# Kernel optimization log

Hardware: AMD Instinct MI355X
Metric: run time of the kernel (lower is better)

## Reference

```python
import jax, jax.numpy as jnp
import numpy as np
import math

D_MODEL = 1024
N_HEADS = 16
FFN_DIM = 4096
B, L = 8, 1024
LN_EPS = 1e-5


def setup_inputs() -> dict:
    key = jax.random.key(0)
    ks = jax.random.split(key, 16)
    s = 1.0 / math.sqrt(D_MODEL)
    sf = 1.0 / math.sqrt(FFN_DIM)
    # weights stored [in, out] (transposed vs torch nn.Linear)
    return {
        "x": jax.random.normal(ks[0], (B, L, D_MODEL), dtype=jnp.float32),
        "Wq": jax.random.normal(ks[1], (D_MODEL, D_MODEL), dtype=jnp.float32) * s,
        "bq": jnp.zeros((D_MODEL,), jnp.float32),
        "Wk": jax.random.normal(ks[2], (D_MODEL, D_MODEL), dtype=jnp.float32) * s,
        "bk": jnp.zeros((D_MODEL,), jnp.float32),
        "Wv": jax.random.normal(ks[3], (D_MODEL, D_MODEL), dtype=jnp.float32) * s,
        "bv": jnp.zeros((D_MODEL,), jnp.float32),
        "Wo": jax.random.normal(ks[4], (D_MODEL, D_MODEL), dtype=jnp.float32) * s,
        "bo": jnp.zeros((D_MODEL,), jnp.float32),
        "W1": jax.random.normal(ks[5], (D_MODEL, FFN_DIM), dtype=jnp.float32) * s,
        "b1": jnp.zeros((FFN_DIM,), jnp.float32),
        "W2": jax.random.normal(ks[6], (FFN_DIM, D_MODEL), dtype=jnp.float32) * sf,
        "b2": jnp.zeros((D_MODEL,), jnp.float32),
        "gamma": jnp.ones((D_MODEL,), jnp.float32),
        "beta": jnp.zeros((D_MODEL,), jnp.float32),
    }


def reference(x, Wq, bq, Wk, bk, Wv, bv, Wo, bo, W1, b1, W2, b2, gamma, beta):
    Bb, Ll, D = x.shape
    H = N_HEADS
    E = D // H
    scale = 1.0 / math.sqrt(E)
    # multi-head attention (dropout is identity in eval)
    q = (x @ Wq + bq).reshape(Bb, Ll, H, E)
    k = (x @ Wk + bk).reshape(Bb, Ll, H, E)
    v = (x @ Wv + bv).reshape(Bb, Ll, H, E)
    scores = jnp.einsum('blhe,bshe->bhls', q, k)  # [B,H,L,L]
    A = jax.nn.softmax(scale * scores, axis=-1)
    ctx = jnp.einsum('bhls,bshd->blhd', A, v).reshape(Bb, Ll, D)
    attn_out = ctx @ Wo + bo
    x = x + attn_out
    # FFN: conv1d kernel_size=1 == pointwise linear; exact (erf) GELU as in F.gelu
    h = jax.nn.gelu(x @ W1 + b1, approximate=False)
    x = x + (h @ W2 + b2)
    # LayerNorm
    mu = jnp.mean(x, axis=-1, keepdims=True)
    var = jnp.mean(jnp.square(x - mu), axis=-1, keepdims=True)
    out = (x - mu) * jax.lax.rsqrt(var + LN_EPS) * gamma + beta
    return out
```

## Files before the change

### kernel.cpp

```cpp
#include <hip/hip_runtime.h>
#include <cmath>

typedef __attribute__((ext_vector_type(8))) _Float16 half8;
typedef __attribute__((ext_vector_type(4))) _Float16 half4;
typedef __attribute__((ext_vector_type(4))) float f32x4;

__device__ __forceinline__ void glds16(const void* g, void* l) {
  __builtin_amdgcn_global_load_lds(
      (__attribute__((address_space(1))) const void*)g,
      (__attribute__((address_space(3))) void*)l, 16, 0, 0);
}

__device__ __forceinline__ float fast_erf(float x) {
  float ax = fabsf(x);
  float t = 1.0f / (1.0f + 0.3275911f * ax);
  float y = t * (0.254829592f +
            t * (-0.284496736f +
            t * (1.421413741f +
            t * (-1.453152027f + t * 1.061405429f))));
  float r = 1.0f - y * __expf(-ax * ax);
  return copysignf(r, x);
}

__global__ __launch_bounds__(256) void k_cvt(const float* __restrict__ in,
                                             _Float16* __restrict__ out) {
  int i = (blockIdx.x * 256 + threadIdx.x) * 8;
  const f32x4* p = (const f32x4*)(in + i);
  f32x4 a = p[0], b = p[1];
  half8 h;
  h[0] = (_Float16)a[0]; h[1] = (_Float16)a[1]; h[2] = (_Float16)a[2]; h[3] = (_Float16)a[3];
  h[4] = (_Float16)b[0]; h[5] = (_Float16)b[1]; h[6] = (_Float16)b[2]; h[7] = (_Float16)b[3];
  *(half8*)(out + i) = h;
}

__global__ __launch_bounds__(256) void k_wt(const float* __restrict__ W,
                                            _Float16* __restrict__ Wt, int K, int N) {
  __shared__ float t[32][33];
  int x = threadIdx.x & 31, y4 = (threadIdx.x >> 5) << 2;
  int n0 = blockIdx.x << 5, k0 = blockIdx.y << 5;
#pragma unroll
  for (int r = 0; r < 4; ++r) t[y4 + r][x] = W[(size_t)(k0 + y4 + r) * N + n0 + x];
  __syncthreads();
#pragma unroll
  for (int r = 0; r < 4; ++r) Wt[(size_t)(n0 + y4 + r) * K + k0 + x] = (_Float16)t[x][y4 + r];
}

__global__ void k_biascat(const float* __restrict__ a, const float* __restrict__ b,
                          const float* __restrict__ c, float* __restrict__ o) {
  int i = blockIdx.x * 256 + threadIdx.x;
  const float* s = i < 1024 ? a : (i < 2048 ? b : c);
  o[i] = s[i & 1023];
}

template <int BM, int EPI>
__global__ __launch_bounds__(512, 2) void k_gemm8(
    const _Float16* __restrict__ A, const _Float16* __restrict__ Bt,
    const float* __restrict__ bias, const float* __restrict__ res,
    float* __restrict__ outf, _Float16* __restrict__ outh, int M, int N, int K) {
  constexpr int MR = BM / 32;
  constexpr int MH2 = MR / 2;
  constexpr int AL = BM * 64;
  constexpr int BL = 256 * 64;
  constexpr int ABYTES = BM * 128;
  constexpr int BBYTES = 256 * 128;
  constexpr int AB2 = 2 * ABYTES;
  __shared__ _Float16 lds[2 * (AL + BL)];
  const char* ldsc = (const char*)lds;

  const int tid = threadIdx.x;
  const int lane = tid & 63;
  const int w = tid >> 6, wr = w >> 2, wc = w & 3;
  const int l15 = lane & 15, grp = lane >> 4;

  const int gx = gridDim.x;
  const int nwg = gx * gridDim.y;
  const int lid = blockIdx.y * gx + blockIdx.x;
  const int wid = (lid & 7) * (nwg >> 3) + (lid >> 3);
  const int m0 = (wid / gx) * BM, n0 = (wid % gx) * 256;

  const int m2 = (l15 >> 2) & 1, m01 = l15 & 3;
  const int chunk0 = (m2 << 2) | (grp ^ m01);
  const int aoff0 = wr * 2048 + l15 * 128 + chunk0 * 16;
  const int aoff1 = aoff0 ^ 64;
  const int boff0 = wc * 2048 + l15 * 128 + chunk0 * 16;
  const int boff1 = boff0 ^ 64;

  const int srow = tid >> 3;
  const int scs8 = ((tid & 7) ^ (srow & 7)) * 8;
  const int NK = K >> 6;

  f32x4 acc[MR][4] = {};
  half8 af[MH2][2], bf[2][2];

#define STG_A(J, MHH, KN)                                                      \
  _Pragma("unroll") for (int s = 0; s < BM / 128; ++s)                         \
      glds16(A + (size_t)(m0 + (MHH) * (BM / 2) + s * 64 + srow) * K +         \
                 (size_t)(KN)*64 + scs8,                                       \
             lds + (J)*AL + ((MHH) * (BM / 2) + s * 64) * 64 + tid * 8);
#define STG_B(J, NHH, KN)                                                      \
  _Pragma("unroll") for (int s = 0; s < 2; ++s)                                \
      glds16(Bt + (size_t)(n0 + (NHH)*128 + s * 64 + srow) * K +               \
                  (size_t)(KN)*64 + scs8,                                      \
             lds + 2 * AL + (J)*BL + ((NHH)*128 + s * 64) * 64 + tid * 8);

#define STG_ALL(J, KN)                                                         \
  STG_A(J, 0, KN) STG_B(J, 0, KN) STG_B(J, 1, KN) STG_A(J, 1, KN)

#define VM_A                                                                   \
  do {                                                                         \
    if constexpr (BM == 256) asm volatile("s_waitcnt vmcnt(8)" ::: "memory");  \
    else asm volatile("s_waitcnt vmcnt(6)" ::: "memory");                      \
  } while (0)
#define VM_B                                                                   \
  do {                                                                         \
    if constexpr (BM == 256) asm volatile("s_waitcnt vmcnt(4)" ::: "memory");  \
    else asm volatile("s_waitcnt vmcnt(3)" ::: "memory");                      \
  } while (0)
#define VM_NONE

#define PHASE(J, MHQ, NHQ, RA, RB, STGSTMT, VMSTMT)                            \
  {                                                                            \
    if constexpr (RA) {                                                        \
      _Pragma("unroll") for (int i = 0; i < MH2; ++i) {                        \
        af[i][0] = *(const half8*)(ldsc + (J)*ABYTES +                         \
                                   ((MHQ)*MH2 + i) * 4096 + aoff0);            \
        af[i][1] = *(const half8*)(ldsc + (J)*ABYTES +                         \
                                   ((MHQ)*MH2 + i) * 4096 + aoff1);            \
      }                                                                        \
    }                                                                          \
    if constexpr (RB) {                                                        \
      _Pragma("unroll") for (int n = 0; n < 2; ++n) {                          \
        bf[n][0] = *(const half8*)(ldsc + AB2 + (J)*BBYTES +                   \
                                   ((NHQ)*2 + n) * 8192 + boff0);              \
        bf[n][1] = *(const half8*)(ldsc + AB2 + (J)*BBYTES +                   \
                                   ((NHQ)*2 + n) * 8192 + boff1);              \
      }                                                                        \
    }                                                                          \
    STGSTMT;                                                                   \
    __builtin_amdgcn_s_barrier();                                              \
    __builtin_amdgcn_s_setprio(1);                                             \
    _Pragma("unroll") for (int ks = 0; ks < 2; ++ks)                           \
        _Pragma("unroll") for (int i = 0; i < MH2; ++i)                        \
            _Pragma("unroll") for (int n = 0; n < 2; ++n)                      \
                acc[(MHQ)*MH2 + i][(NHQ)*2 + n] =                              \
                    __builtin_amdgcn_mfma_f32_16x16x32_f16(                    \
                        af[i][ks], bf[n][ks], acc[(MHQ)*MH2 + i][(NHQ)*2 + n], \
                        0, 0, 0);                                              \
    __builtin_amdgcn_s_setprio(0);                                             \
    VMSTMT;                                                                    \
    __builtin_amdgcn_s_barrier();                                              \
  }

#define KTILE(J, KT)                                                           \
  {                                                                            \
    const int kn_ = ((KT) + 1 < NK) ? (KT) + 1 : (KT);                         \
    PHASE(J, 0, 0, true, true, STG_ALL(1 - (J), kn_), VM_A)                    \
    PHASE(J, 0, 1, false, true, , VM_NONE)                                     \
    PHASE(J, 1, 1, true, false, , VM_NONE)                                     \
    PHASE(J, 1, 0, false, true, , VM_B)                                        \
  }

  STG_ALL(0, 0)
  VM_B;
  __builtin_amdgcn_s_barrier();

#pragma unroll 1
  for (int kt = 0; kt < NK; kt += 2) {
    KTILE(0, kt)
    KTILE(1, kt + 1)
  }
  asm volatile("s_waitcnt vmcnt(0)" ::: "memory");
#undef KTILE
#undef PHASE
#undef VM_A
#undef VM_B
#undef VM_NONE
#undef STG_ALL
#undef STG_A
#undef STG_B

  float bcol[4];
#pragma unroll
  for (int n = 0; n < 4; ++n) bcol[n] = bias[n0 + (n * 4 + wc) * 16 + l15];
#pragma unroll
  for (int m = 0; m < MR; ++m) {
#pragma unroll
    for (int rr = 0; rr < 4; ++rr) {
      const size_t row = m0 + (m * 2 + wr) * 16 + grp * 4 + rr;
#pragma unroll
      for (int n = 0; n < 4; ++n) {
        const int col = n0 + (n * 4 + wc) * 16 + l15;
        float v = acc[m][n][rr] + bcol[n];
        const size_t idx = row * N + col;
        if (EPI == 0) {
          outh[idx] = (_Float16)v;
        } else if (EPI == 1) {
          float t2 = v + res[idx];
          outf[idx] = t2;
          outh[idx] = (_Float16)t2;
        } else if (EPI == 2) {
          float g = 0.5f * v * (1.0f + fast_erf(v * 0.70710678118654752f));
          outh[idx] = (_Float16)g;
        } else {
          outf[idx] = v + res[idx];
        }
      }
    }
  }
}

__global__ __launch_bounds__(256) void k_vt(const _Float16* __restrict__ qkv,
                                            _Float16* __restrict__ Vt) {
  __shared__ _Float16 t[64 * 66];
  const int tid = threadIdx.x;
  const int bh = blockIdx.y, b = bh >> 4, h = bh & 15;
  const int s0 = blockIdx.x << 6;
#pragma unroll
  for (int p = 0; p < 2; ++p) {
    int lin = p * 256 + tid;
    int s = lin >> 3, c8 = lin & 7;
    half8 v = *(const half8*)&qkv[(size_t)(b * 1024 + s0 + s) * 3072 + 2048 + h * 64 + c8 * 8];
    union { half8 h8; unsigned u[4]; } u;
    u.h8 = v;
    unsigned* d = (unsigned*)&t[s * 66 + c8 * 8];
#pragma unroll
    for (int k = 0; k < 4; ++k) d[k] = u.u[k];
  }
  __syncthreads();
#pragma unroll
  for (int p = 0; p < 2; ++p) {
    int lin = p * 256 + tid;
    int e = lin >> 3, c8 = lin & 7;
    half8 v;
#pragma unroll
    for (int j = 0; j < 8; ++j) v[j] = t[(c8 * 8 + j) * 66 + e];
    *(half8*)&Vt[(size_t)(bh * 64 + e) * 1024 + s0 + c8 * 8] = v;
  }
}

__global__ __launch_bounds__(256) void k_attn(const _Float16* __restrict__ qkv,
                                              const _Float16* __restrict__ Vt,
                                              _Float16* __restrict__ ctx) {
  __shared__ _Float16 Ks[128 * 64];
  __shared__ _Float16 Vs[64 * 128];
  __shared__ _Float16 Ps[4][16 * 136];
  const int tid = threadIdx.x;
  const int lane = tid & 63, w = tid >> 6;
  const int l15 = lane & 15, grp = lane >> 4;
  const int bh = blockIdx.y, b = bh >> 4, h = bh & 15;
  const int q0 = blockIdx.x << 6;
  const float CSC = 0.125f * 1.44269504088896f;

  half8 qf[2];
  {
    const _Float16* qp = qkv + (size_t)(b * 1024 + q0 + w * 16 + l15) * 3072 + h * 64 + grp * 8;
    qf[0] = *(const half8*)qp;
    qf[1] = *(const half8*)(qp + 32);
  }
  f32x4 octx[4] = {};
  float mrun = -1e30f, lrun = 0.f;

  for (int kt = 0; kt < 8; ++kt) {
    const int s0 = kt * 128;
#pragma unroll
    for (int i = 0; i < 4; ++i) {
      {
        int srow = i * 32 + (tid >> 3);
        int c8 = (tid & 7) ^ (srow & 7);
        glds16(qkv + (size_t)(b * 1024 + s0 + srow) * 3072 + 1024 + h * 64 + c8 * 8,
               Ks + w * 512 + i * 2048);
      }
      {
        int erow = i * 16 + (tid >> 4);
        int c16 = (tid & 15) ^ (erow & 7);
        glds16(Vt + (size_t)(bh * 64 + erow) * 1024 + s0 + c16 * 8,
               Vs + w * 512 + i * 2048);
      }
    }
    __syncthreads();
    f32x4 sacc[8] = {};
#pragma unroll
    for (int ks = 0; ks < 2; ++ks)
#pragma unroll
      for (int f = 0; f < 8; ++f) {
        int srow = f * 16 + l15;
        half8 kf = *(const half8*)&Ks[srow * 64 + ((ks * 32 + grp * 8) ^ ((srow & 7) * 8))];
        sacc[f] = __builtin_amdgcn_mfma_f32_16x16x32_f16(kf, qf[ks], sacc[f], 0, 0, 0);
      }
    float sv[8][4];
    float tmax = -1e30f;
#pragma unroll
    for (int f = 0; f < 8; ++f)
#pragma unroll
      for (int r = 0; r < 4; ++r) {
        float v = sacc[f][r] * CSC;
        sv[f][r] = v;
        tmax = fmaxf(tmax, v);
      }
    tmax = fmaxf(tmax, __shfl_xor(tmax, 16));
    tmax = fmaxf(tmax, __shfl_xor(tmax, 32));
    float mnew = fmaxf(mrun, tmax);
    float corr = exp2f(mrun - mnew);
    float tsum = 0.f;
#pragma unroll
    for (int f = 0; f < 8; ++f)
#pragma unroll
      for (int r = 0; r < 4; ++r) {
        float pv = exp2f(sv[f][r] - mnew);
        sv[f][r] = pv;
        tsum += pv;
      }
    tsum += __shfl_xor(tsum, 16);
    tsum += __shfl_xor(tsum, 32);
    lrun = lrun * corr + tsum;
    mrun = mnew;
#pragma unroll
    for (int r = 0; r < 4; ++r) {
      float cq = __shfl(corr, (lane & 48) + grp * 4 + r);
#pragma unroll
      for (int jf = 0; jf < 4; ++jf) octx[jf][r] *= cq;
    }
#pragma unroll
    for (int f = 0; f < 8; ++f) {
      half4 pk;
      pk[0] = (_Float16)sv[f][0]; pk[1] = (_Float16)sv[f][1];
      pk[2] = (_Float16)sv[f][2]; pk[3] = (_Float16)sv[f][3];
      *(half4*)&Ps[w][l15 * 136 + f * 16 + grp * 4] = pk;
    }
#pragma unroll
    for (int ks2 = 0; ks2 < 4; ++ks2) {
      half8 pa = *(const half8*)&Ps[w][l15 * 136 + ks2 * 32 + grp * 8];
#pragma unroll
      for (int jf = 0; jf < 4; ++jf) {
        int erow = jf * 16 + l15;
        half8 vb = *(const half8*)&Vs[erow * 128 + ((ks2 * 32 + grp * 8) ^ ((erow & 7) * 8))];
        octx[jf] = __builtin_amdgcn_mfma_f32_16x16x32_f16(pa, vb, octx[jf], 0, 0, 0);
      }
    }
    __syncthreads();
  }
#pragma unroll
  for (int r = 0; r < 4; ++r) {
    float lq = __shfl(lrun, (lane & 48) + grp * 4 + r);
    float inv = 1.0f / lq;
    const size_t row = b * 1024 + q0 + w * 16 + grp * 4 + r;
#pragma unroll
    for (int jf = 0; jf < 4; ++jf)
      ctx[row * 1024 + h * 64 + jf * 16 + l15] = (_Float16)(octx[jf][r] * inv);
  }
}

__global__ __launch_bounds__(256) void k_ln(const float* xin, const float* __restrict__ gamma,
                                            const float* __restrict__ beta, float* out) {
  __shared__ float red[8];
  const int tid = threadIdx.x;
  const size_t row = blockIdx.x;
  f32x4 v = *(const f32x4*)&xin[row * 1024 + tid * 4];
  float s = v[0] + v[1] + v[2] + v[3];
  float s2 = v[0] * v[0] + v[1] * v[1] + v[2] * v[2] + v[3] * v[3];
#pragma unroll
  for (int o = 32; o >= 1; o >>= 1) {
    s += __shfl_xor(s, o);
    s2 += __shfl_xor(s2, o);
  }
  if ((tid & 63) == 0) { red[tid >> 6] = s; red[4 + (tid >> 6)] = s2; }
  __syncthreads();
  s = red[0] + red[1] + red[2] + red[3];
  s2 = red[4] + red[5] + red[6] + red[7];
  float mu = s * (1.0f / 1024.0f);
  float var = s2 * (1.0f / 1024.0f) - mu * mu;
  float rs = rsqrtf(var + 1e-5f);
  f32x4 g = *(const f32x4*)&gamma[tid * 4];
  f32x4 bt = *(const f32x4*)&beta[tid * 4];
  f32x4 o4;
#pragma unroll
  for (int r = 0; r < 4; ++r) o4[r] = (v[r] - mu) * rs * g[r] + bt[r];
  *(f32x4*)&out[row * 1024 + tid * 4] = o4;
}

extern "C" void kernel_launch(void* const* d_in, const int* in_sizes, int n_in,
                              void* d_out, int out_size, void* d_ws, size_t ws_size,
                              hipStream_t stream) {
  (void)in_sizes; (void)n_in; (void)out_size; (void)ws_size;
  const float* x  = (const float*)d_in[0];
  const float* Wq = (const float*)d_in[1];  const float* bq = (const float*)d_in[2];
  const float* Wk = (const float*)d_in[3];  const float* bk = (const float*)d_in[4];
  const float* Wv = (const float*)d_in[5];  const float* bv = (const float*)d_in[6];
  const float* Wo = (const float*)d_in[7];  const float* bo = (const float*)d_in[8];
  const float* W1 = (const float*)d_in[9];  const float* b1 = (const float*)d_in[10];
  const float* W2 = (const float*)d_in[11]; const float* b2 = (const float*)d_in[12];
  const float* gamma = (const float*)d_in[13];
  const float* beta  = (const float*)d_in[14];
  float* out = (float*)d_out;

  char* p = (char*)d_ws;
  _Float16* xb    = (_Float16*)p;  p += (size_t)16 << 20;
  _Float16* qkv   = (_Float16*)p;
  _Float16* hbuf  = (_Float16*)p;  p += (size_t)48 << 20;
  _Float16* Vt    = (_Float16*)p;  p += (size_t)16 << 20;
  _Float16* Wqkvt = (_Float16*)p;  p += (size_t)3072 * 1024 * 2;
  _Float16* Wot   = (_Float16*)p;  p += (size_t)1024 * 1024 * 2;
  _Float16* W1t   = (_Float16*)p;  p += (size_t)4096 * 1024 * 2;
  _Float16* W2t   = (_Float16*)p;  p += (size_t)4096 * 1024 * 2;
  float*    bqkv  = (float*)p;     p += (size_t)3072 * 4;
  float*    x1    = (float*)p;     p += (size_t)32 << 20;
  _Float16* x1b   = (_Float16*)p;  p += (size_t)16 << 20;
  _Float16* ctx   = xb;

  k_cvt<<<4096, 256, 0, stream>>>(x, xb);
  k_wt<<<dim3(32, 32), 256, 0, stream>>>(Wq, Wqkvt, 1024, 1024);
  k_wt<<<dim3(32, 32), 256, 0, stream>>>(Wk, Wqkvt + 1024 * 1024, 1024, 1024);
  k_wt<<<dim3(32, 32), 256, 0, stream>>>(Wv, Wqkvt + 2048 * 1024, 1024, 1024);
  k_wt<<<dim3(32, 32), 256, 0, stream>>>(Wo, Wot, 1024, 1024);
  k_wt<<<dim3(128, 32), 256, 0, stream>>>(W1, W1t, 1024, 4096);
  k_wt<<<dim3(32, 128), 256, 0, stream>>>(W2, W2t, 4096, 1024);
  k_biascat<<<12, 256, 0, stream>>>(bq, bk, bv, bqkv);

  k_gemm8<128, 0><<<dim3(12, 64), 512, 0, stream>>>(xb, Wqkvt, bqkv, nullptr, nullptr, qkv,
                                                    8192, 3072, 1024);
  k_vt<<<dim3(16, 128), 256, 0, stream>>>(qkv, Vt);
  k_attn<<<dim3(16, 128), 256, 0, stream>>>(qkv, Vt, ctx);
  k_gemm8<128, 1><<<dim3(4, 64), 512, 0, stream>>>(ctx, Wot, bo, x, x1, x1b, 8192, 1024, 1024);
  k_gemm8<256, 2><<<dim3(16, 32), 512, 0, stream>>>(x1b, W1t, b1, nullptr, nullptr, hbuf,
                                                    8192, 4096, 1024);
  k_gemm8<128, 3><<<dim3(4, 64), 512, 0, stream>>>(hbuf, W2t, b2, x1, out, nullptr,
                                                   8192, 1024, 4096);
  k_ln<<<8192, 256, 0, stream>>>(out, gamma, beta, out);
}
```

Before: 380.0 us.

## Add triple-buffered 256x128 GEMM kernel for QKV, out-proj and FFN2

Introduces k_gemmf, a 256x128-tile GEMM with three LDS stages and a two-tile-ahead global-to-LDS prefetch, two workgroups per CU, and an XCD-aware block remap. It replaces the older 128-row k_gemm8 for the QKV, output-projection and second FFN GEMMs. The aim is deeper load/compute overlap and better L2 locality. It also adds an explicit lgkmcnt wait and sched_barrier before the MFMA block, and hardcodes the vmcnt waits in the existing kernel to the BM=256 values. That kernel is now only instantiated with BM=256, so the hardcoding is consistent. The larger LDS footprint and the extra waits could limit occupancy or add stalls.

```diff
diff --git a/kernel.cpp b/kernel.cpp
--- a/kernel.cpp
+++ b/kernel.cpp
@@ -106,16 +106,8 @@
 #define STG_ALL(J, KN)                                                         \
   STG_A(J, 0, KN) STG_B(J, 0, KN) STG_B(J, 1, KN) STG_A(J, 1, KN)
 
-#define VM_A                                                                   \
-  do {                                                                         \
-    if constexpr (BM == 256) asm volatile("s_waitcnt vmcnt(8)" ::: "memory");  \
-    else asm volatile("s_waitcnt vmcnt(6)" ::: "memory");                      \
-  } while (0)
-#define VM_B                                                                   \
-  do {                                                                         \
-    if constexpr (BM == 256) asm volatile("s_waitcnt vmcnt(4)" ::: "memory");  \
-    else asm volatile("s_waitcnt vmcnt(3)" ::: "memory");                      \
-  } while (0)
+#define VM_A asm volatile("s_waitcnt vmcnt(8)" ::: "memory")
+#define VM_B asm volatile("s_waitcnt vmcnt(4)" ::: "memory")
 #define VM_NONE
 
 #define PHASE(J, MHQ, NHQ, RA, RB, STGSTMT, VMSTMT)                            \
@@ -138,6 +130,8 @@
     }                                                                          \
     STGSTMT;                                                                   \
     __builtin_amdgcn_s_barrier();                                              \
+    asm volatile("s_waitcnt lgkmcnt(0)");                                      \
+    __builtin_amdgcn_sched_barrier(0);                                         \
     __builtin_amdgcn_s_setprio(1);                                             \
     _Pragma("unroll") for (int ks = 0; ks < 2; ++ks)                           \
         _Pragma("unroll") for (int i = 0; i < MH2; ++i)                        \
@@ -209,6 +203,124 @@
   }
 }
 
+template <int EPI>
+__global__ __launch_bounds__(512, 2) void k_gemmf(
+    const _Float16* __restrict__ A, const _Float16* __restrict__ Bt,
+    const float* __restrict__ bias, const float* __restrict__ res,
+    float* __restrict__ outf, _Float16* __restrict__ outh, int M, int N, int K) {
+  constexpr int AL = 256 * 64, BL = 128 * 64;
+  constexpr int ABY = 32768, BBY = 16384, BBASE = 3 * ABY;
+  __shared__ _Float16 lds[3 * (AL + BL)];
+  const char* ldsc = (const char*)lds;
+
+  const int tid = threadIdx.x;
+  const int lane = tid & 63;
+  const int w = tid >> 6, wr = w >> 1, wc = w & 1;
+  const int l15 = lane & 15, grp = lane >> 4;
+
+  const int gx = gridDim.x;
+  const int nwg = gx * gridDim.y;
+  const int lid = blockIdx.y * gx + blockIdx.x;
+  const int wid = (lid & 7) * (nwg >> 3) + (lid >> 3);
+  const int m0 = (wid / gx) * 256, n0 = (wid % gx) * 128;
+
+  const int m2 = (l15 >> 2) & 1, m01 = l15 & 3;
+  const int c0 = ((m2 << 2) | (grp ^ m01)) * 16;
+  const int aoff0 = wr * 2048 + l15 * 128 + c0;
+  const int aoff1 = aoff0 ^ 64;
+  const int boff0 = wc * 2048 + l15 * 128 + c0;
+  const int boff1 = boff0 ^ 64;
+
+  const int srow = tid >> 3;
+  const int scs8 = ((tid & 7) ^ (srow & 7)) * 8;
+  const int NK = K >> 6;
+
+  const _Float16* aG = A + (size_t)(m0 + srow) * K + scs8;
+  const _Float16* bG = Bt + (size_t)(n0 + srow) * K + scs8;
+
+  f32x4 acc[4][4] = {};
+
+#define FSTG_A(JJ, HH, KN)                                                     \
+  _Pragma("unroll") for (int s = 0; s < 2; ++s)                                \
+      glds16(aG + (size_t)((HH)*128 + s * 64) * K + (size_t)(KN)*64,           \
+             lds + (JJ)*AL + ((HH)*128 + s * 64) * 64 + tid * 8);
+#define FSTG_B(JJ, HH, KN)                                                     \
+  glds16(bG + (size_t)((HH)*64) * K + (size_t)(KN)*64,                         \
+         lds + 3 * AL + (JJ)*BL + (HH)*64 * 64 + tid * 8);
+
+#define FPHASE(PA, PB, AO, BO, STGSTMT, VMSTMT)                                \
+  {                                                                            \
+    half8 af_[4], bf_[4];                                                      \
+    _Pragma("unroll") for (int m = 0; m < 4; ++m)                              \
+        af_[m] = *(const half8*)((PA) + m * 8192 + (AO));                      \
+    _Pragma("unroll") for (int n = 0; n < 4; ++n)                              \
+        bf_[n] = *(const half8*)((PB) + n * 4096 + (BO));                      \
+    STGSTMT;                                                                   \
+    __builtin_amdgcn_s_barrier();                                              \
+    asm volatile("s_waitcnt lgkmcnt(0)");                                      \
+    __builtin_amdgcn_sched_barrier(0);                                         \
+    __builtin_amdgcn_s_setprio(1);                                             \
+    _Pragma("unroll") for (int m = 0; m < 4; ++m)                              \
+        _Pragma("unroll") for (int n = 0; n < 4; ++n)                          \
+            acc[m][n] = __builtin_amdgcn_mfma_f32_16x16x32_f16(                \
+                af_[m], bf_[n], acc[m][n], 0, 0, 0);                           \
+    __builtin_amdgcn_s_setprio(0);                                             \
+    VMSTMT;                                                                    \
+    __builtin_amdgcn_s_barrier();                                              \
+  }
+
+  FSTG_A(0, 0, 0) FSTG_A(0, 1, 0) FSTG_B(0, 0, 0) FSTG_B(0, 1, 0)
+  FSTG_A(1, 0, 1) FSTG_A(1, 1, 1) FSTG_B(1, 0, 1) FSTG_B(1, 1, 1)
+  asm volatile("s_waitcnt vmcnt(6)" ::: "memory");
+  __builtin_amdgcn_s_barrier();
+
+  int j = 0, j2 = 2;
+#pragma unroll 1
+  for (int kt = 0; kt < NK; ++kt) {
+    const int kn = (kt + 2 < NK) ? kt + 2 : NK - 1;
+    const char* pa = ldsc + j * ABY;
+    const char* pb = ldsc + BBASE + j * BBY;
+    FPHASE(pa, pb, aoff0, boff0, { FSTG_A(j2, 0, kn) FSTG_B(j2, 0, kn) }, )
+    FPHASE(pa, pb, aoff1, boff1, { FSTG_A(j2, 1, kn) FSTG_B(j2, 1, kn) },
+           asm volatile("s_waitcnt vmcnt(6)" ::: "memory");)
+    j = (j == 2) ? 0 : j + 1;
+    j2 = (j2 == 2) ? 0 : j2 + 1;
+  }
+  asm volatile("s_waitcnt vmcnt(0)" ::: "memory");
+#undef FPHASE
+#undef FSTG_A
+#undef FSTG_B
+
+  float bcol[4];
+#pragma unroll
+  for (int n = 0; n < 4; ++n) bcol[n] = bias[n0 + (n * 2 + wc) * 16 + l15];
+#pragma unroll
+  for (int m = 0; m < 4; ++m) {
+#pragma unroll
+    for (int rr = 0; rr < 4; ++rr) {
+      const size_t row = m0 + (m * 4 + wr) * 16 + grp * 4 + rr;
+#pragma unroll
+      for (int n = 0; n < 4; ++n) {
+        const int col = n0 + (n * 2 + wc) * 16 + l15;
+        float v = acc[m][n][rr] + bcol[n];
+        const size_t idx = row * N + col;
+        if (EPI == 0) {
+          outh[idx] = (_Float16)v;
+        } else if (EPI == 1) {
+          float t2 = v + res[idx];
+          outf[idx] = t2;
+          outh[idx] = (_Float16)t2;
+        } else if (EPI == 2) {
+          float g = 0.5f * v * (1.0f + fast_erf(v * 0.70710678118654752f));
+          outh[idx] = (_Float16)g;
+        } else {
+          outf[idx] = v + res[idx];
+        }
+      }
+    }
+  }
+}
+
 __global__ __launch_bounds__(256) void k_vt(const _Float16* __restrict__ qkv,
                                             _Float16* __restrict__ Vt) {
   __shared__ _Float16 t[64 * 66];
@@ -416,14 +528,14 @@
   k_wt<<<dim3(32, 128), 256, 0, stream>>>(W2, W2t, 4096, 1024);
   k_biascat<<<12, 256, 0, stream>>>(bq, bk, bv, bqkv);
 
-  k_gemm8<128, 0><<<dim3(12, 64), 512, 0, stream>>>(xb, Wqkvt, bqkv, nullptr, nullptr, qkv,
-                                                    8192, 3072, 1024);
+  k_gemmf<0><<<dim3(24, 32), 512, 0, stream>>>(xb, Wqkvt, bqkv, nullptr, nullptr, qkv,
+                                               8192, 3072, 1024);
   k_vt<<<dim3(16, 128), 256, 0, stream>>>(qkv, Vt);
   k_attn<<<dim3(16, 128), 256, 0, stream>>>(qkv, Vt, ctx);
-  k_gemm8<128, 1><<<dim3(4, 64), 512, 0, stream>>>(ctx, Wot, bo, x, x1, x1b, 8192, 1024, 1024);
+  k_gemmf<1><<<dim3(8, 32), 512, 0, stream>>>(ctx, Wot, bo, x, x1, x1b, 8192, 1024, 1024);
   k_gemm8<256, 2><<<dim3(16, 32), 512, 0, stream>>>(x1b, W1t, b1, nullptr, nullptr, hbuf,
                                                     8192, 4096, 1024);
-  k_gemm8<128, 3><<<dim3(4, 64), 512, 0, stream>>>(hbuf, W2t, b2, x1, out, nullptr,
-                                                   8192, 1024, 4096);
+  k_gemmf<3><<<dim3(8, 32), 512, 0, stream>>>(hbuf, W2t, b2, x1, out, nullptr,
+                                              8192, 1024, 4096);
   k_ln<<<8192, 256, 0, stream>>>(out, gamma, beta, out);
 }
```

Measured after the change: 373.0 us. No clear change (-1.8%).
